# Kernel tuning notes

Hardware: AMD Instinct MI355X
Metric: run time of the kernel (lower is better)

The kernel has to match this reference:

```python
import jax, jax.numpy as jnp
import numpy as np

E, D, H, O, K = 12, 1024, 2048, 1024, 4
HH, G1, G2 = H // 2, 256, 128
B = 4096


def _ln(x, g, b):
    # torch LayerNorm over last dim, eps=1e-5
    m = x.mean(-1, keepdims=True)
    v = ((x - m) ** 2).mean(-1, keepdims=True)
    return (x - m) * jax.lax.rsqrt(v + 1e-5) * g + b


def setup_inputs() -> dict:
    key = jax.random.key(0)
    ks = jax.random.split(key, 12)
    s = 0.02
    f32 = jnp.float32
    return {
        "x": jax.random.normal(ks[0], (B, D), f32),
        # stacked expert params (E experts)
        "ew_in": jax.random.normal(ks[1], (E, D, H), f32) * s,
        "eb_in": jnp.full((E, H), 0.1, f32),
        "ln1_g": jnp.ones((E, H), f32),
        "ln1_b": jnp.zeros((E, H), f32),
        "ew_h1": jax.random.normal(ks[2], (E, H, H), f32) * s,
        "eb_h1": jnp.full((E, H), 0.1, f32),
        "ln2_g": jnp.ones((E, H), f32),
        "ln2_b": jnp.zeros((E, H), f32),
        "ew_h2": jax.random.normal(ks[3], (E, H, HH), f32) * s,
        "eb_h2": jnp.full((E, HH), 0.1, f32),
        "ew_out": jax.random.normal(ks[4], (E, HH, O), f32) * s,
        "eb_out": jnp.zeros((E, O), f32),
        # gating network params
        "gw_in": jax.random.normal(ks[5], (D, G1), f32) * s,
        "gb_in": jnp.zeros((G1,), f32),
        "gln1_g": jnp.ones((G1,), f32),
        "gln1_b": jnp.zeros((G1,), f32),
        "gw_1": jax.random.normal(ks[6], (G1, G1), f32) * s,
        "gb_1": jnp.full((G1,), 0.1, f32),
        "gln2_g": jnp.ones((G1,), f32),
        "gln2_b": jnp.zeros((G1,), f32),
        "gw_2": jax.random.normal(ks[7], (G1, G2), f32) * s,
        "gb_2": jnp.full((G2,), 0.1, f32),
        "gw_out": jax.random.normal(ks[8], (G2, E), f32) * s,
        "gb_out": jnp.zeros((E,), f32),
        "temperature": jnp.ones((1,), f32),
    }


def _moe(x, ew_in, eb_in, ln1_g, ln1_b, ew_h1, eb_h1, ln2_g, ln2_b, ew_h2,
         eb_h2, ew_out, eb_out, gw_in, gb_in, gln1_g, gln1_b, gw_1, gb_1,
         gln2_g, gln2_b, gw_2, gb_2, gw_out, gb_out, temperature):
    # ---- gating network (eval mode: no dropout / noise) ----
    g0 = jax.nn.relu(x @ gw_in + gb_in)                                # [B,256]
    g1 = jax.nn.relu(_ln(g0, gln1_g, gln1_b)) @ gw_1 + gb_1 + g0       # residual
    g2 = jax.nn.relu(_ln(g1, gln2_g, gln2_b)) @ gw_2 + gb_2            # [B,128]
    logits = (g2 @ gw_out + gb_out) / temperature                      # [B,E]
    probs = jax.nn.softmax(logits, axis=1)
    topp, topi = jax.lax.top_k(probs, K)                               # [B,K]
    topp = topp / topp.sum(axis=1, keepdims=True)
    # ---- experts: batched over E, combined with top-k one-hot weights ----
    h0 = jax.nn.relu(jnp.einsum('bd,edh->ebh', x, ew_in) + eb_in[:, None, :])
    a1 = jax.nn.relu(_ln(h0, ln1_g[:, None, :], ln1_b[:, None, :]))
    h1 = jnp.einsum('ebh,ehg->ebg', a1, ew_h1) + eb_h1[:, None, :] + h0
    a2 = jax.nn.silu(_ln(h1, ln2_g[:, None, :], ln2_b[:, None, :]))
    h2 = jnp.einsum('ebh,ehm->ebm', a2, ew_h2) + eb_h2[:, None, :]     # [E,B,H/2]
    y = jnp.einsum('ebm,emo->ebo', h2, ew_out) + eb_out[:, None, :]    # [E,B,O]
    oh = jax.nn.one_hot(topi, E, dtype=probs.dtype)                    # [B,K,E]
    w = jnp.einsum('bk,bke->be', topp, oh)                             # combine weights
    final = jnp.einsum('be,ebo->bo', w, y)                             # [B,O]
    # ---- load-balancing loss (eval-mode path) ----
    usage = probs.mean(axis=0)                                         # [E]
    ideal = 1.0 / E
    kl = jnp.sum(ideal * (jnp.log(ideal) - jnp.log(usage + 1e-8)))
    var = jnp.sum((usage - ideal) ** 2)
    ent = -jnp.sum(usage * jnp.log(usage + 1e-8))
    ent_loss = 1.0 - ent / np.log(E).astype(np.float32)
    loss = (0.5 * kl + 0.3 * var + 0.2 * ent_loss) * 0.05
    return final, loss, probs


def reference(x, ew_in, eb_in, ln1_g, ln1_b, ew_h1, eb_h1, ln2_g, ln2_b,
              ew_h2, eb_h2, ew_out, eb_out, gw_in, gb_in, gln1_g, gln1_b,
              gw_1, gb_1, gln2_g, gln2_b, gw_2, gb_2, gw_out, gb_out,
              temperature):
    return _moe(x, ew_in, eb_in, ln1_g, ln1_b, ew_h1, eb_h1, ln2_g, ln2_b,
                ew_h2, eb_h2, ew_out, eb_out, gw_in, gb_in, gln1_g, gln1_b,
                gw_1, gb_1, gln2_g, gln2_b, gw_2, gb_2, gw_out, gb_out,
                temperature)
```

## Files before the change

kernel.cpp:

```cpp
#include <hip/hip_runtime.h>
#include <cstdint>
#include <cstddef>

typedef __bf16 bf16;
typedef __bf16 bf16x4 __attribute__((ext_vector_type(4)));
typedef __bf16 bf16x8 __attribute__((ext_vector_type(8)));
typedef float  f32x4  __attribute__((ext_vector_type(4)));

#define NE   12
#define DDIM 1024
#define HDIM 2048
#define MDIM 1024
#define ODIM 1024
#define GG1  256
#define GG2  128
#define BB   4096
#define ROWS_MAX 18432

#define GPTR(p) ((const __attribute__((address_space(1))) void*)(p))
#define LPTR(p) ((__attribute__((address_space(3))) void*)(p))

__global__ void cvt_f32_bf16(const float* __restrict__ in, bf16* __restrict__ out) {
    size_t i = ((size_t)blockIdx.x * 256 + threadIdx.x) * 4;
    float4 v = *(const float4*)(in + i);
    bf16x4 o = { (bf16)v.x, (bf16)v.y, (bf16)v.z, (bf16)v.w };
    *(bf16x4*)(out + i) = o;
}

__global__ __launch_bounds__(256)
void transpose_cvt(const float* __restrict__ in, bf16* __restrict__ out,
                   int K, int N) {
    __shared__ float tile[64][65];
    const size_t eo = (size_t)blockIdx.z * K * N;
    in  += eo;
    out += eo;
    const int n0 = blockIdx.x * 64, k0 = blockIdx.y * 64;
    const int tid = threadIdx.x;

    const int rkk = tid >> 4, rnc = (tid & 15) * 4;
    #pragma unroll
    for (int p = 0; p < 4; ++p) {
        const int kk = p * 16 + rkk;
        const float4 v = *(const float4*)(in + (size_t)(k0 + kk) * N + n0 + rnc);
        tile[kk][rnc] = v.x; tile[kk][rnc + 1] = v.y;
        tile[kk][rnc + 2] = v.z; tile[kk][rnc + 3] = v.w;
    }
    __syncthreads();

    const int wnn = tid >> 3, wkc = (tid & 7) * 8;
    #pragma unroll
    for (int p = 0; p < 2; ++p) {
        const int nn = p * 32 + wnn;
        bf16x8 o;
        #pragma unroll
        for (int j = 0; j < 8; ++j) o[j] = (bf16)tile[wkc + j][nn];
        *(bf16x8*)(out + (size_t)(n0 + nn) * K + k0 + wkc) = o;
    }
}

__global__ void route_init(int* __restrict__ tok2slot, int* __restrict__ lists,
                           int* __restrict__ counts, int* __restrict__ cursors) {
    const int i = blockIdx.x * 256 + threadIdx.x;
    if (i < BB * NE)   tok2slot[i] = -1;
    if (i < ROWS_MAX)  lists[i] = 0;
    if (i < NE)        { counts[i] = 0; cursors[i] = 0; }
}

__global__ void route_count(const float* __restrict__ wcomb, int* __restrict__ counts) {
    const int t = blockIdx.x * 256 + threadIdx.x;
    const int e = blockIdx.y;
    if (wcomb[(size_t)t * NE + e] > 0.f) atomicAdd(&counts[e], 1);
}

__global__ void route_offsets(const int* __restrict__ counts, int* __restrict__ offs) {
    if (threadIdx.x == 0) {
        int o = 0;
        for (int e = 0; e < NE; ++e) { offs[e] = o; o += (counts[e] + 127) & ~127; }
        offs[NE] = o;
    }
}

__global__ void route_assign(const float* __restrict__ wcomb, const int* __restrict__ offs,
                             int* __restrict__ cursors, int* __restrict__ lists,
                             int* __restrict__ tok2slot) {
    const int t = blockIdx.x * 256 + threadIdx.x;
    const int e = blockIdx.y;
    if (wcomb[(size_t)t * NE + e] > 0.f) {
        const int pos  = atomicAdd(&cursors[e], 1);
        const int slot = offs[e] + pos;
        lists[slot] = t;
        tok2slot[(size_t)t * NE + e] = slot;
    }
}

__global__ void combine_out(const int* __restrict__ tok2slot, const float* __restrict__ wcomb,
                            const float* __restrict__ yc, float* __restrict__ out) {
    const int t = blockIdx.x, tid = threadIdx.x;
    float4 acc = { 0.f, 0.f, 0.f, 0.f };
    #pragma unroll
    for (int e = 0; e < NE; ++e) {
        const int s = tok2slot[(size_t)t * NE + e];
        if (s >= 0) {
            const float w = wcomb[(size_t)t * NE + e];
            const float4 y = *(const float4*)&yc[(size_t)s * ODIM + tid * 4];
            acc.x += w * y.x; acc.y += w * y.y; acc.z += w * y.z; acc.w += w * y.w;
        }
    }
    *(float4*)&out[(size_t)t * ODIM + tid * 4] = acc;
}

template<int EPI>
__global__ __launch_bounds__(256, 2)
void egemm(const bf16* __restrict__ A, const bf16* __restrict__ Wt,
           const float* __restrict__ bias, const bf16* __restrict__ res,
           bf16* __restrict__ Cb, float* __restrict__ Cf,
           const int* __restrict__ offs, const int* __restrict__ lists,
           int N, int K)
{
    const int e = blockIdx.z;
    const int off  = offs[e];
    const int cntp = offs[e + 1] - off;
    const int m0 = blockIdx.y * 128;
    if (m0 >= cntp) return;
    const int n0 = blockIdx.x * 128;

    __shared__ bf16 sA[3][128 * 32];
    __shared__ bf16 sB[3][128 * 32];
    const int tid  = threadIdx.x;
    const int lane = tid & 63;
    const int wave = tid >> 6;
    const int wr = wave >> 1, wc = wave & 1;
    const int q  = lane >> 4;
    const int lr = lane & 15;

    const bf16*  Wte = Wt + (size_t)e * N * K;
    const float* be  = bias + (size_t)e * N;

    const bf16* srcA[2];
    const bf16* srcB[2];
    int dsto[2];
    #pragma unroll
    for (int i = 0; i < 2; ++i) {
        const int ch  = i * 256 + tid;
        const int row = ch >> 2, c = ch & 3;
        const int qg  = c ^ ((row >> 1) & 3);
        size_t arow;
        if constexpr (EPI == 0) arow = (size_t)lists[off + m0 + row];
        else                    arow = (size_t)(off + m0 + row);
        srcA[i] = A   + arow * K + qg * 8;
        srcB[i] = Wte + (size_t)(n0 + row) * K + qg * 8;
        dsto[i] = (i * 256 + (tid & 192)) * 8;
    }

    f32x4 acc[4][4] = {};

    auto stage = [&](int buf, int kt) {
        const int k0 = kt << 5;
        #pragma unroll
        for (int i = 0; i < 2; ++i) {
            __builtin_amdgcn_global_load_lds(GPTR(srcA[i] + k0), LPTR(&sA[buf][dsto[i]]), 16, 0, 0);
            __builtin_amdgcn_global_load_lds(GPTR(srcB[i] + k0), LPTR(&sB[buf][dsto[i]]), 16, 0, 0);
        }
    };

    const int NT = K >> 5;
    stage(0, 0);
    stage(1, 1);

    for (int kt = 0; kt < NT; ++kt) {
        const int cur = kt % 3;
        if (kt + 1 < NT) { asm volatile("s_waitcnt vmcnt(4)" ::: "memory"); }
        else             { asm volatile("s_waitcnt vmcnt(0)" ::: "memory"); }
        __builtin_amdgcn_sched_barrier(0);
        __builtin_amdgcn_s_barrier();
        __builtin_amdgcn_sched_barrier(0);

        bf16x8 fa[4], fb[4];
        #pragma unroll
        for (int mi = 0; mi < 4; ++mi) {
            const int r = wr * 64 + mi * 16 + lr;
            const int c = q ^ ((r >> 1) & 3);
            fa[mi] = *(const bf16x8*)&sA[cur][(size_t)(r * 4 + c) * 8];
        }
        #pragma unroll
        for (int ni = 0; ni < 4; ++ni) {
            const int r = wc * 64 + ni * 16 + lr;
            const int c = q ^ ((r >> 1) & 3);
            fb[ni] = *(const bf16x8*)&sB[cur][(size_t)(r * 4 + c) * 8];
        }
        #pragma unroll
        for (int mi = 0; mi < 4; ++mi)
            #pragma unroll
            for (int ni = 0; ni < 4; ++ni)
                acc[mi][ni] = __builtin_amdgcn_mfma_f32_16x16x32_bf16(fa[mi], fb[ni], acc[mi][ni], 0, 0, 0);

        if (kt + 2 < NT) stage((kt + 2) % 3, kt + 2);
    }

    #pragma unroll
    for (int ni = 0; ni < 4; ++ni) {
        const int c  = n0 + wc * 64 + ni * 16 + lr;
        const float bv = be[c];
        #pragma unroll
        for (int mi = 0; mi < 4; ++mi) {
            const int rloc = wr * 64 + mi * 16 + q * 4;
            #pragma unroll
            for (int j = 0; j < 4; ++j) {
                const size_t idx = (size_t)(off + m0 + rloc + j) * N + c;
                float v = acc[mi][ni][j] + bv;
                if constexpr (EPI == 0)      { Cb[idx] = (bf16)fmaxf(v, 0.f); }
                else if constexpr (EPI == 1) { Cb[idx] = (bf16)(v + (float)res[idx]); }
                else if constexpr (EPI == 2) { Cb[idx] = (bf16)v; }
                else                         { Cf[idx] = v; }
            }
        }
    }
}

template<int ACT>
__global__ __launch_bounds__(256)
void ln_act_bf16(const bf16* __restrict__ in, const float* __restrict__ gam,
                 const float* __restrict__ bet, bf16* __restrict__ out,
                 const int* __restrict__ offs)
{
    const int e = blockIdx.y;
    const int row = blockIdx.x;
    const int off = offs[e];
    if (row >= offs[e + 1] - off) return;
    const int tid = threadIdx.x;
    const size_t base = (size_t)(off + row) * HDIM;
    const float* g = gam + (size_t)e * HDIM;
    const float* b = bet + (size_t)e * HDIM;
    bf16x8 v = *(const bf16x8*)(in + base + tid * 8);
    float x[8], s = 0.f, ss = 0.f;
    #pragma unroll
    for (int j = 0; j < 8; ++j) { x[j] = (float)v[j]; s += x[j]; ss += x[j] * x[j]; }
    #pragma unroll
    for (int o = 1; o < 64; o <<= 1) { s += __shfl_xor(s, o); ss += __shfl_xor(ss, o); }
    __shared__ float rs[4], rss[4];
    if ((tid & 63) == 0) { rs[tid >> 6] = s; rss[tid >> 6] = ss; }
    __syncthreads();
    s  = rs[0] + rs[1] + rs[2] + rs[3];
    ss = rss[0] + rss[1] + rss[2] + rss[3];
    const float mean = s * (1.f / HDIM);
    const float var  = ss * (1.f / HDIM) - mean * mean;
    const float rstd = rsqrtf(var + 1e-5f);
    bf16x8 ov;
    #pragma unroll
    for (int j = 0; j < 8; ++j) {
        const int col = tid * 8 + j;
        float y = (x[j] - mean) * rstd * g[col] + b[col];
        if constexpr (ACT == 0) y = fmaxf(y, 0.f);
        else                    y = y / (1.f + expf(-y));
        ov[j] = (bf16)y;
    }
    *(bf16x8*)(out + base + tid * 8) = ov;
}

template<int EPI>
__global__ __launch_bounds__(256)
void gemm_f32(const float* __restrict__ A, const float* __restrict__ Bm,
              const float* __restrict__ bias, const float* __restrict__ res,
              float* __restrict__ C, int M, int N, int K)
{
    __shared__ float As[64][17];
    __shared__ float Bs[16][64];
    const int tid = threadIdx.x;
    const int tx = tid & 15, ty = tid >> 4;
    const int n0 = blockIdx.x * 64, m0 = blockIdx.y * 64;
    float acc[4][4] = {};

    for (int k0 = 0; k0 < K; k0 += 16) {
        {
            const int r = tid >> 2, c = (tid & 3) * 4;
            const float4 va = *(const float4*)(A + (size_t)(m0 + r) * K + k0 + c);
            As[r][c] = va.x; As[r][c + 1] = va.y; As[r][c + 2] = va.z; As[r][c + 3] = va.w;
            const int rb = tid >> 4, cb = (tid & 15) * 4;
            *(float4*)&Bs[rb][cb] = *(const float4*)(Bm + (size_t)(k0 + rb) * N + n0 + cb);
        }
        __syncthreads();
        #pragma unroll
        for (int k = 0; k < 16; ++k) {
            const float4 b4 = *(const float4*)&Bs[k][tx * 4];
            float av[4];
            #pragma unroll
            for (int i = 0; i < 4; ++i) av[i] = As[ty * 4 + i][k];
            #pragma unroll
            for (int i = 0; i < 4; ++i) {
                acc[i][0] += av[i] * b4.x; acc[i][1] += av[i] * b4.y;
                acc[i][2] += av[i] * b4.z; acc[i][3] += av[i] * b4.w;
            }
        }
        __syncthreads();
    }

    const float4 b4 = *(const float4*)(bias + n0 + tx * 4);
    #pragma unroll
    for (int i = 0; i < 4; ++i) {
        const int r = m0 + ty * 4 + i;
        float o[4] = { acc[i][0] + b4.x, acc[i][1] + b4.y, acc[i][2] + b4.z, acc[i][3] + b4.w };
        if constexpr (EPI == 0) {
            #pragma unroll
            for (int j = 0; j < 4; ++j) o[j] = fmaxf(o[j], 0.f);
        } else if constexpr (EPI == 1) {
            const float4 r4 = *(const float4*)(res + (size_t)r * N + n0 + tx * 4);
            o[0] += r4.x; o[1] += r4.y; o[2] += r4.z; o[3] += r4.w;
        }
        float4 o4 = { o[0], o[1], o[2], o[3] };
        *(float4*)(C + (size_t)r * N + n0 + tx * 4) = o4;
    }
}

__global__ __launch_bounds__(256)
void gemm_f32_sk(const float* __restrict__ A, const float* __restrict__ Bm,
                 float* __restrict__ Cp, int M, int N, int K)
{
    __shared__ float As[64][17];
    __shared__ float Bs[16][64];
    const int tid = threadIdx.x;
    const int tx = tid & 15, ty = tid >> 4;
    const int n0 = blockIdx.x * 64, m0 = blockIdx.y * 64;
    const int kh = K >> 1;
    const int kb = blockIdx.z * kh, ke = kb + kh;
    float acc[4][4] = {};

    for (int k0 = kb; k0 < ke; k0 += 16) {
        {
            const int r = tid >> 2, c = (tid & 3) * 4;
            const float4 va = *(const float4*)(A + (size_t)(m0 + r) * K + k0 + c);
            As[r][c] = va.x; As[r][c + 1] = va.y; As[r][c + 2] = va.z; As[r][c + 3] = va.w;
            const int rb = tid >> 4, cb = (tid & 15) * 4;
            *(float4*)&Bs[rb][cb] = *(const float4*)(Bm + (size_t)(k0 + rb) * N + n0 + cb);
        }
        __syncthreads();
        #pragma unroll
        for (int k = 0; k < 16; ++k) {
            const float4 b4 = *(const float4*)&Bs[k][tx * 4];
            float av[4];
            #pragma unroll
            for (int i = 0; i < 4; ++i) av[i] = As[ty * 4 + i][k];
            #pragma unroll
            for (int i = 0; i < 4; ++i) {
                acc[i][0] += av[i] * b4.x; acc[i][1] += av[i] * b4.y;
                acc[i][2] += av[i] * b4.z; acc[i][3] += av[i] * b4.w;
            }
        }
        __syncthreads();
    }

    float* Cz = Cp + (size_t)blockIdx.z * M * N;
    #pragma unroll
    for (int i = 0; i < 4; ++i) {
        const int r = m0 + ty * 4 + i;
        float4 o4 = { acc[i][0], acc[i][1], acc[i][2], acc[i][3] };
        *(float4*)(Cz + (size_t)r * N + n0 + tx * 4) = o4;
    }
}

__global__ void sk_reduce_relu(const float* __restrict__ Cp, const float* __restrict__ bias,
                               float* __restrict__ C)
{
    const size_t i = ((size_t)blockIdx.x * 256 + threadIdx.x) * 4;
    const int col = (int)(i % GG1);
    const float4 a = *(const float4*)(Cp + i);
    const float4 b = *(const float4*)(Cp + (size_t)BB * GG1 + i);
    const float4 bi = *(const float4*)(bias + col);
    float4 o;
    o.x = fmaxf(a.x + b.x + bi.x, 0.f);
    o.y = fmaxf(a.y + b.y + bi.y, 0.f);
    o.z = fmaxf(a.z + b.z + bi.z, 0.f);
    o.w = fmaxf(a.w + b.w + bi.w, 0.f);
    *(float4*)(C + i) = o;
}

__global__ void ln_relu_f32_256(const float* __restrict__ in, const float* __restrict__ g,
                                const float* __restrict__ b, float* __restrict__ out)
{
    const int row = blockIdx.x, lane = threadIdx.x;
    const size_t base = (size_t)row * GG1;
    const float4 v = *(const float4*)(in + base + lane * 4);
    float s  = v.x + v.y + v.z + v.w;
    float ss = v.x * v.x + v.y * v.y + v.z * v.z + v.w * v.w;
    #pragma unroll
    for (int o = 1; o < 64; o <<= 1) { s += __shfl_xor(s, o); ss += __shfl_xor(ss, o); }
    const float mean = s * (1.f / GG1);
    const float var  = ss * (1.f / GG1) - mean * mean;
    const float rstd = rsqrtf(var + 1e-5f);
    const float4 g4 = *(const float4*)(g + lane * 4);
    const float4 b4 = *(const float4*)(b + lane * 4);
    float4 o4;
    o4.x = fmaxf((v.x - mean) * rstd * g4.x + b4.x, 0.f);
    o4.y = fmaxf((v.y - mean) * rstd * g4.y + b4.y, 0.f);
    o4.z = fmaxf((v.z - mean) * rstd * g4.z + b4.z, 0.f);
    o4.w = fmaxf((v.w - mean) * rstd * g4.w + b4.w, 0.f);
    *(float4*)(out + base + lane * 4) = o4;
}

__global__ void gate_head(const float* __restrict__ g2, const float* __restrict__ gwout,
                          const float* __restrict__ gbout, const float* __restrict__ temp,
                          float* __restrict__ probs_out, float* __restrict__ wout)
{
    const int row = blockIdx.x, lane = threadIdx.x;
    __shared__ float lg[NE];
    const int e = lane >> 2, part = lane & 3;
    float acc = 0.f;
    if (e < NE) {
        const float* gr = g2 + (size_t)row * GG2;
        #pragma unroll
        for (int i = 0; i < 32; ++i) {
            const int k = part * 32 + i;
            acc += gr[k] * gwout[(size_t)k * NE + e];
        }
    }
    acc += __shfl_xor(acc, 1);
    acc += __shfl_xor(acc, 2);
    if (e < NE && part == 0) lg[e] = acc + gbout[e];
    __syncthreads();
    if (lane == 0) {
        const float t = temp[0];
        float p[NE];
        float mx = -1e30f;
        #pragma unroll
        for (int i = 0; i < NE; ++i) { p[i] = lg[i] / t; mx = fmaxf(mx, p[i]); }
        float se = 0.f;
        #pragma unroll
        for (int i = 0; i < NE; ++i) { p[i] = expf(p[i] - mx); se += p[i]; }
        const float inv = 1.f / se;
        #pragma unroll
        for (int i = 0; i < NE; ++i) { p[i] *= inv; probs_out[(size_t)row * NE + i] = p[i]; }
        float qq[NE], w[NE];
        #pragma unroll
        for (int i = 0; i < NE; ++i) { qq[i] = p[i]; w[i] = 0.f; }
        float tv[4]; int ti[4]; float tsum = 0.f;
        for (int k = 0; k < 4; ++k) {
            int best = 0; float bv = qq[0];
            for (int i = 1; i < NE; ++i) if (qq[i] > bv) { bv = qq[i]; best = i; }
            tv[k] = bv; ti[k] = best; qq[best] = -1e30f; tsum += bv;
        }
        const float it = 1.f / tsum;
        for (int k = 0; k < 4; ++k) w[ti[k]] = tv[k] * it;
        #pragma unroll
        for (int i = 0; i < NE; ++i) wout[(size_t)row * NE + i] = w[i];
    }
}

__global__ void usage_mean(const float* __restrict__ probs, float* __restrict__ usage) {
    const int e = blockIdx.x, tid = threadIdx.x;
    float s = 0.f;
    for (int r = tid; r < BB; r += 256) s += probs[(size_t)r * NE + e];
    #pragma unroll
    for (int o = 1; o < 64; o <<= 1) s += __shfl_xor(s, o);
    __shared__ float ps[4];
    if ((tid & 63) == 0) ps[tid >> 6] = s;
    __syncthreads();
    if (tid == 0) usage[e] = (ps[0] + ps[1] + ps[2] + ps[3]) / (float)BB;
}

__global__ void loss_kernel(const float* __restrict__ usage, float* __restrict__ out_loss) {
    if (threadIdx.x == 0) {
        const float ideal = 1.f / 12.f;
        float kl = 0.f, var = 0.f, ent = 0.f;
        for (int e = 0; e < NE; ++e) {
            const float u = usage[e];
            kl  += ideal * (logf(ideal) - logf(u + 1e-8f));
            var += (u - ideal) * (u - ideal);
            ent -= u * logf(u + 1e-8f);
        }
        const float entl = 1.f - ent / logf(12.f);
        out_loss[0] = (0.5f * kl + 0.3f * var + 0.2f * entl) * 0.05f;
    }
}

extern "C" void kernel_launch(void* const* d_in, const int* in_sizes, int n_in,
                              void* d_out, int out_size, void* d_ws, size_t ws_size,
                              hipStream_t stream)
{
    const float* x      = (const float*)d_in[0];
    const float* ew_in  = (const float*)d_in[1];
    const float* eb_in  = (const float*)d_in[2];
    const float* ln1_g  = (const float*)d_in[3];
    const float* ln1_b  = (const float*)d_in[4];
    const float* ew_h1  = (const float*)d_in[5];
    const float* eb_h1  = (const float*)d_in[6];
    const float* ln2_g  = (const float*)d_in[7];
    const float* ln2_b  = (const float*)d_in[8];
    const float* ew_h2  = (const float*)d_in[9];
    const float* eb_h2  = (const float*)d_in[10];
    const float* ew_out = (const float*)d_in[11];
    const float* eb_out = (const float*)d_in[12];
    const float* gw_in  = (const float*)d_in[13];
    const float* gb_in  = (const float*)d_in[14];
    const float* gln1_g = (const float*)d_in[15];
    const float* gln1_b = (const float*)d_in[16];
    const float* gw_1   = (const float*)d_in[17];
    const float* gb_1   = (const float*)d_in[18];
    const float* gln2_g = (const float*)d_in[19];
    const float* gln2_b = (const float*)d_in[20];
    const float* gw_2   = (const float*)d_in[21];
    const float* gb_2   = (const float*)d_in[22];
    const float* gw_out = (const float*)d_in[23];
    const float* gb_out = (const float*)d_in[24];
    const float* temp   = (const float*)d_in[25];

    float* out_final = (float*)d_out;
    float* out_loss  = out_final + (size_t)BB * ODIM;
    float* out_probs = out_loss + 1;

    char* ws = (char*)d_ws;
    size_t off = 0;
    auto alloc = [&](size_t bytes) -> void* {
        void* p = ws + off;
        off += (bytes + 255) & ~(size_t)255;
        return p;
    };

    bf16* xb     = (bf16*)alloc((size_t)BB * DDIM * 2);
    bf16* wt_in  = (bf16*)alloc((size_t)NE * HDIM * DDIM * 2);
    bf16* wt_h1  = (bf16*)alloc((size_t)NE * HDIM * HDIM * 2);
    bf16* wt_h2  = (bf16*)alloc((size_t)NE * MDIM * HDIM * 2);
    bf16* wt_out = (bf16*)alloc((size_t)NE * ODIM * MDIM * 2);
    bf16* regA   = (bf16*)alloc((size_t)ROWS_MAX * HDIM * 2);
    bf16* regB   = (bf16*)alloc((size_t)ROWS_MAX * HDIM * 2);
    bf16* h1     = (bf16*)alloc((size_t)ROWS_MAX * HDIM * 2);
    float* yc    = (float*)alloc((size_t)ROWS_MAX * ODIM * 4);
    bf16* h0 = regA; bf16* a2 = regA;
    bf16* a1 = regB; bf16* h2 = regB;
    float* skbuf = (float*)alloc((size_t)2 * BB * GG1 * 4);
    float* g0    = (float*)alloc((size_t)BB * GG1 * 4);
    float* t1    = (float*)alloc((size_t)BB * GG1 * 4);
    float* g1    = (float*)alloc((size_t)BB * GG1 * 4);
    float* t2    = (float*)alloc((size_t)BB * GG1 * 4);
    float* g2b   = (float*)alloc((size_t)BB * GG2 * 4);
    float* wcomb = (float*)alloc((size_t)BB * NE * 4);
    int*   lists = (int*)alloc((size_t)ROWS_MAX * 4);
    int*   t2s   = (int*)alloc((size_t)BB * NE * 4);
    int*   counts= (int*)alloc(256);
    int*   curs  = (int*)alloc(256);
    int*   offs  = (int*)alloc(256);
    float* usage = (float*)alloc(256);

    cvt_f32_bf16<<<dim3(BB * DDIM / 1024), dim3(256), 0, stream>>>(x, xb);
    transpose_cvt<<<dim3(HDIM / 64, DDIM / 64, NE), dim3(256), 0, stream>>>(ew_in,  wt_in,  DDIM, HDIM);
    transpose_cvt<<<dim3(HDIM / 64, HDIM / 64, NE), dim3(256), 0, stream>>>(ew_h1,  wt_h1,  HDIM, HDIM);
    transpose_cvt<<<dim3(MDIM / 64, HDIM / 64, NE), dim3(256), 0, stream>>>(ew_h2,  wt_h2,  HDIM, MDIM);
    transpose_cvt<<<dim3(ODIM / 64, MDIM / 64, NE), dim3(256), 0, stream>>>(ew_out, wt_out, MDIM, ODIM);

    gemm_f32_sk<<<dim3(GG1 / 64, BB / 64, 2), dim3(256), 0, stream>>>(x, gw_in, skbuf, BB, GG1, DDIM);
    sk_reduce_relu<<<dim3(BB * GG1 / 1024), dim3(256), 0, stream>>>(skbuf, gb_in, g0);
    ln_relu_f32_256<<<dim3(BB), dim3(64), 0, stream>>>(g0, gln1_g, gln1_b, t1);
    gemm_f32<1><<<dim3(GG1 / 64, BB / 64), dim3(256), 0, stream>>>(t1, gw_1,  gb_1,  g0,      g1,  BB, GG1, GG1);
    ln_relu_f32_256<<<dim3(BB), dim3(64), 0, stream>>>(g1, gln2_g, gln2_b, t2);
    gemm_f32<2><<<dim3(GG2 / 64, BB / 64), dim3(256), 0, stream>>>(t2, gw_2,  gb_2,  nullptr, g2b, BB, GG2, GG1);
    gate_head<<<dim3(BB), dim3(64), 0, stream>>>(g2b, gw_out, gb_out, temp, out_probs, wcomb);
    usage_mean<<<dim3(NE), dim3(256), 0, stream>>>(out_probs, usage);
    loss_kernel<<<dim3(1), dim3(64), 0, stream>>>(usage, out_loss);

    route_init<<<dim3((BB * NE + 255) / 256), dim3(256), 0, stream>>>(t2s, lists, counts, curs);
    route_count<<<dim3(BB / 256, NE), dim3(256), 0, stream>>>(wcomb, counts);
    route_offsets<<<dim3(1), dim3(64), 0, stream>>>(counts, offs);
    route_assign<<<dim3(BB / 256, NE), dim3(256), 0, stream>>>(wcomb, offs, curs, lists, t2s);

    egemm<0><<<dim3(HDIM / 128, BB / 128, NE), dim3(256), 0, stream>>>(
        xb, wt_in, eb_in, nullptr, h0, nullptr, offs, lists, HDIM, DDIM);
    ln_act_bf16<0><<<dim3(BB, NE), dim3(256), 0, stream>>>(h0, ln1_g, ln1_b, a1, offs);
    egemm<1><<<dim3(HDIM / 128, BB / 128, NE), dim3(256), 0, stream>>>(
        a1, wt_h1, eb_h1, h0, h1, nullptr, offs, lists, HDIM, HDIM);
    ln_act_bf16<1><<<dim3(BB, NE), dim3(256), 0, stream>>>(h1, ln2_g, ln2_b, a2, offs);
    egemm<2><<<dim3(MDIM / 128, BB / 128, NE), dim3(256), 0, stream>>>(
        a2, wt_h2, eb_h2, nullptr, h2, nullptr, offs, lists, MDIM, HDIM);
    egemm<3><<<dim3(ODIM / 128, BB / 128, NE), dim3(256), 0, stream>>>(
        h2, wt_out, eb_out, nullptr, nullptr, yc, offs, lists, ODIM, MDIM);

    combine_out<<<dim3(BB), dim3(256), 0, stream>>>(t2s, wcomb, yc, out_final);
}
```

Baseline: 853.1 us.

## Fuse weighted expert combine into final expert GEMM epilogue via atomics

Stores each slot's gate weight next to the token list, so the last expert GEMM scales its output and atomically adds it into the final output. This removes the fp32 per-slot output buffer, the tok2slot table and the separate combine kernel. In exchange it adds a memset of the output and scattered fp32 atomic adds, up to K per element, whose order is nondeterministic. Padding slots are skipped by checking for a zero weight.

```diff
diff --git a/kernel.cpp b/kernel.cpp
--- a/kernel.cpp
+++ b/kernel.cpp
@@ -58,12 +58,11 @@
     }
 }
 
-__global__ void route_init(int* __restrict__ tok2slot, int* __restrict__ lists,
+__global__ void route_init(int* __restrict__ lists, float* __restrict__ wlists,
                            int* __restrict__ counts, int* __restrict__ cursors) {
     const int i = blockIdx.x * 256 + threadIdx.x;
-    if (i < BB * NE)   tok2slot[i] = -1;
-    if (i < ROWS_MAX)  lists[i] = 0;
-    if (i < NE)        { counts[i] = 0; cursors[i] = 0; }
+    if (i < ROWS_MAX) { lists[i] = 0; wlists[i] = 0.f; }
+    if (i < NE)       { counts[i] = 0; cursors[i] = 0; }
 }
 
 __global__ void route_count(const float* __restrict__ wcomb, int* __restrict__ counts) {
@@ -82,31 +81,16 @@
 
 __global__ void route_assign(const float* __restrict__ wcomb, const int* __restrict__ offs,
                              int* __restrict__ cursors, int* __restrict__ lists,
-                             int* __restrict__ tok2slot) {
+                             float* __restrict__ wlists) {
     const int t = blockIdx.x * 256 + threadIdx.x;
     const int e = blockIdx.y;
-    if (wcomb[(size_t)t * NE + e] > 0.f) {
+    const float w = wcomb[(size_t)t * NE + e];
+    if (w > 0.f) {
         const int pos  = atomicAdd(&cursors[e], 1);
         const int slot = offs[e] + pos;
-        lists[slot] = t;
-        tok2slot[(size_t)t * NE + e] = slot;
-    }
-}
-
-__global__ void combine_out(const int* __restrict__ tok2slot, const float* __restrict__ wcomb,
-                            const float* __restrict__ yc, float* __restrict__ out) {
-    const int t = blockIdx.x, tid = threadIdx.x;
-    float4 acc = { 0.f, 0.f, 0.f, 0.f };
-    #pragma unroll
-    for (int e = 0; e < NE; ++e) {
-        const int s = tok2slot[(size_t)t * NE + e];
-        if (s >= 0) {
-            const float w = wcomb[(size_t)t * NE + e];
-            const float4 y = *(const float4*)&yc[(size_t)s * ODIM + tid * 4];
-            acc.x += w * y.x; acc.y += w * y.y; acc.z += w * y.z; acc.w += w * y.w;
-        }
-    }
-    *(float4*)&out[(size_t)t * ODIM + tid * 4] = acc;
+        lists[slot]  = t;
+        wlists[slot] = w;
+    }
 }
 
 template<int EPI>
@@ -115,7 +99,7 @@
            const float* __restrict__ bias, const bf16* __restrict__ res,
            bf16* __restrict__ Cb, float* __restrict__ Cf,
            const int* __restrict__ offs, const int* __restrict__ lists,
-           int N, int K)
+           const float* __restrict__ wlists, int N, int K)
 {
     const int e = blockIdx.z;
     const int off  = offs[e];
@@ -206,12 +190,20 @@
             const int rloc = wr * 64 + mi * 16 + q * 4;
             #pragma unroll
             for (int j = 0; j < 4; ++j) {
-                const size_t idx = (size_t)(off + m0 + rloc + j) * N + c;
+                const int slot = off + m0 + rloc + j;
                 float v = acc[mi][ni][j] + bv;
-                if constexpr (EPI == 0)      { Cb[idx] = (bf16)fmaxf(v, 0.f); }
-                else if constexpr (EPI == 1) { Cb[idx] = (bf16)(v + (float)res[idx]); }
-                else if constexpr (EPI == 2) { Cb[idx] = (bf16)v; }
-                else                         { Cf[idx] = v; }
+                if constexpr (EPI == 3) {
+                    const float wl = wlists[slot];
+                    if (wl > 0.f) {
+                        const int t = lists[slot];
+                        atomicAdd(&Cf[(size_t)t * N + c], wl * v);
+                    }
+                } else {
+                    const size_t idx = (size_t)slot * N + c;
+                    if constexpr (EPI == 0)      { Cb[idx] = (bf16)fmaxf(v, 0.f); }
+                    else if constexpr (EPI == 1) { Cb[idx] = (bf16)(v + (float)res[idx]); }
+                    else                         { Cb[idx] = (bf16)v; }
+                }
             }
         }
     }
@@ -522,7 +514,6 @@
     bf16* regA   = (bf16*)alloc((size_t)ROWS_MAX * HDIM * 2);
     bf16* regB   = (bf16*)alloc((size_t)ROWS_MAX * HDIM * 2);
     bf16* h1     = (bf16*)alloc((size_t)ROWS_MAX * HDIM * 2);
-    float* yc    = (float*)alloc((size_t)ROWS_MAX * ODIM * 4);
     bf16* h0 = regA; bf16* a2 = regA;
     bf16* a1 = regB; bf16* h2 = regB;
     float* skbuf = (float*)alloc((size_t)2 * BB * GG1 * 4);
@@ -533,7 +524,7 @@
     float* g2b   = (float*)alloc((size_t)BB * GG2 * 4);
     float* wcomb = (float*)alloc((size_t)BB * NE * 4);
     int*   lists = (int*)alloc((size_t)ROWS_MAX * 4);
-    int*   t2s   = (int*)alloc((size_t)BB * NE * 4);
+    float* wlists= (float*)alloc((size_t)ROWS_MAX * 4);
     int*   counts= (int*)alloc(256);
     int*   curs  = (int*)alloc(256);
     int*   offs  = (int*)alloc(256);
@@ -555,21 +546,21 @@
     usage_mean<<<dim3(NE), dim3(256), 0, stream>>>(out_probs, usage);
     loss_kernel<<<dim3(1), dim3(64), 0, stream>>>(usage, out_loss);
 
-    route_init<<<dim3((BB * NE + 255) / 256), dim3(256), 0, stream>>>(t2s, lists, counts, curs);
+    route_init<<<dim3((ROWS_MAX + 255) / 256), dim3(256), 0, stream>>>(lists, wlists, counts, curs);
     route_count<<<dim3(BB / 256, NE), dim3(256), 0, stream>>>(wcomb, counts);
     route_offsets<<<dim3(1), dim3(64), 0, stream>>>(counts, offs);
-    route_assign<<<dim3(BB / 256, NE), dim3(256), 0, stream>>>(wcomb, offs, curs, lists, t2s);
+    route_assign<<<dim3(BB / 256, NE), dim3(256), 0, stream>>>(wcomb, offs, curs, lists, wlists);
+
+    hipMemsetAsync(out_final, 0, (size_t)BB * ODIM * 4, stream);
 
     egemm<0><<<dim3(HDIM / 128, BB / 128, NE), dim3(256), 0, stream>>>(
-        xb, wt_in, eb_in, nullptr, h0, nullptr, offs, lists, HDIM, DDIM);
+        xb, wt_in, eb_in, nullptr, h0, nullptr, offs, lists, wlists, HDIM, DDIM);
     ln_act_bf16<0><<<dim3(BB, NE), dim3(256), 0, stream>>>(h0, ln1_g, ln1_b, a1, offs);
     egemm<1><<<dim3(HDIM / 128, BB / 128, NE), dim3(256), 0, stream>>>(
-        a1, wt_h1, eb_h1, h0, h1, nullptr, offs, lists, HDIM, HDIM);
+        a1, wt_h1, eb_h1, h0, h1, nullptr, offs, lists, wlists, HDIM, HDIM);
     ln_act_bf16<1><<<dim3(BB, NE), dim3(256), 0, stream>>>(h1, ln2_g, ln2_b, a2, offs);
     egemm<2><<<dim3(MDIM / 128, BB / 128, NE), dim3(256), 0, stream>>>(
-        a2, wt_h2, eb_h2, nullptr, h2, nullptr, offs, lists, MDIM, HDIM);
+        a2, wt_h2, eb_h2, nullptr, h2, nullptr, offs, lists, wlists, MDIM, HDIM);
     egemm<3><<<dim3(ODIM / 128, BB / 128, NE), dim3(256), 0, stream>>>(
-        h2, wt_out, eb_out, nullptr, nullptr, yc, offs, lists, ODIM, MDIM);
-
-    combine_out<<<dim3(BB), dim3(256), 0, stream>>>(t2s, wcomb, yc, out_final);
-}
+        h2, wt_out, eb_out, nullptr, nullptr, out_final, offs, lists, wlists, ODIM, MDIM);
+}
```

After: 905.3 us. +6.1%, slower.
